# Kernel tuning notes

Measured on AMD Instinct MI355X. Metric: run time of the kernel, lower is better.

The kernel has to match this reference:

```python
import jax, jax.numpy as jnp
import numpy as np

B, H, W, C, F, K = 64, 56, 56, 256, 256, 3


def _conv(x, w, padding):
    # NHWC input, HWIO kernel, stride 1
    return jax.lax.conv_general_dilated(
        x, w, window_strides=(1, 1), padding=padding,
        dimension_numbers=('NHWC', 'HWIO', 'NHWC'))


def setup_inputs() -> dict:
    key = jax.random.key(0)
    kx, kw = jax.random.split(key)
    x = jax.random.normal(kx, (B, H, W, C), dtype=jnp.float32)
    stdv = 1.0 / np.sqrt(K * K * C)  # matches build()'s init scale
    w = (jax.random.normal(kw, (K, K, C, F), dtype=jnp.float32) * stdv).astype(jnp.float32)
    return {"x": x, "w": w}


def reference(x, w):
    # fp16_grad forward: round-trip weights through fp16
    wq = w.astype(jnp.float16).astype(jnp.float32)
    # binarize_weight forward value: sign(clip(w, -1, 1))
    wb = jnp.sign(jnp.clip(wq, -1.0, 1.0))
    return _conv(x, wb, 'SAME')
```

## Files before the change

kernel.cpp:

```cpp
#include <hip/hip_runtime.h>
#include <hip/hip_bf16.h>
#include <hip/hip_fp16.h>

typedef __bf16 bf16x8 __attribute__((ext_vector_type(8)));
typedef float  f32x4  __attribute__((ext_vector_type(4)));

#define C_H 56
#define C_W 56
#define C_C 256
#define C_F 256
#define C_B 64
#define N_PIX (C_B * C_H * C_W)
#define WB_ELEMS (9 * C_C * C_F)
#define WB_BYTES (WB_ELEMS * 2)
#define ZBUF_BYTES 1024
#define XB_OFF (WB_BYTES + ZBUF_BYTES)
#define X_ELEMS (N_PIX * C_C)

#define GLOAD_LDS16(g, l)                                                   \
    __builtin_amdgcn_global_load_lds(                                        \
        (const __attribute__((address_space(1))) void*)(g),                  \
        (__attribute__((address_space(3))) void*)(l), 16, 0, 0)

__global__ void prep_w_kernel(const float* __restrict__ w, __bf16* __restrict__ wbT) {
    int idx = blockIdx.x * 256 + threadIdx.x;
    int f = idx & 255;
    int c = (idx >> 8) & 255;
    int s = idx >> 16;
    float wf = w[idx];
    float v = __half2float(__float2half(wf));
    float sgn = (v > 0.f) ? 1.f : ((v < 0.f) ? -1.f : 0.f);
    wbT[(s << 16) + (f << 8) + c] = (__bf16)sgn;
}

__global__ void zero_kernel(float* __restrict__ z) {
    z[threadIdx.x] = 0.f;
}

__global__ void prep_x_kernel(const float* __restrict__ x, __bf16* __restrict__ xb) {
    int i = blockIdx.x * 256 + threadIdx.x;
    const f32x4* p = reinterpret_cast<const f32x4*>(x) + (size_t)i * 2;
    f32x4 a = p[0], b = p[1];
    bf16x8 o;
    o[0] = (__bf16)a[0]; o[1] = (__bf16)a[1]; o[2] = (__bf16)a[2]; o[3] = (__bf16)a[3];
    o[4] = (__bf16)b[0]; o[5] = (__bf16)b[1]; o[6] = (__bf16)b[2]; o[7] = (__bf16)b[3];
    reinterpret_cast<bf16x8*>(xb)[i] = o;
}

__global__ __launch_bounds__(512, 2) void conv_mfma8_kernel(
    const char* __restrict__ xbp,
    const char* __restrict__ wbp,
    const char* __restrict__ zp,
    float* __restrict__ out) {

    __shared__ __align__(16) char sm[4][32768];

    const int nbid = (blockIdx.x & 7) * 98 + (blockIdx.x >> 3);
    const long m0 = (long)nbid * 256;

    const int tid  = threadIdx.x;
    const int lane = tid & 63;
    const int wave = tid >> 6;
    const int l15  = lane & 15;
    const int g4   = lane >> 4;
    const int wm   = wave >> 2;
    const int wn   = wave & 3;
    const int colr = ((g4 ^ (l15 & 3)) << 4);

    const int r0 = tid >> 2;
    const int sw = (((tid & 3) << 4)) ^ ((r0 & 3) << 4);
    const int p0 = (int)m0 + r0;
    const int p1 = p0 + 128;
    const int rem0 = p0 % 3136;
    const int rem1 = p1 % 3136;
    const int y0 = rem0 / 56, x0 = rem0 - (rem0 / 56) * 56;
    const int y1 = rem1 / 56, x1 = rem1 - (rem1 / 56) * 56;

    auto stage = [&](int kts) {
        int cc = (kts * 57) >> 9;
        int s  = kts - 9 * cc;
        int s3 = (s * 171) >> 9;
        int dy = s3 - 1;
        int dx = s - 3 * s3 - 1;
        int doff = dy * 56 + dx;
        size_t cb = (size_t)(cc << 6) + sw;
        bool v0 = ((unsigned)(y0 + dy) < 56u) & ((unsigned)(x0 + dx) < 56u);
        bool v1 = ((unsigned)(y1 + dy) < 56u) & ((unsigned)(x1 + dx) < 56u);
        const char* a0 = v0 ? xbp + (size_t)(p0 + doff) * 512 + cb : zp + sw;
        const char* a1 = v1 ? xbp + (size_t)(p1 + doff) * 512 + cb : zp + sw;
        const char* b0 = wbp + (size_t)((s << 8) + r0) * 512 + cb;
        const char* b1 = wbp + (size_t)((s << 8) + r0 + 128) * 512 + cb;
        char* L = &sm[kts & 3][0];
        GLOAD_LDS16(a0, L + tid * 16);
        GLOAD_LDS16(a1, L + 8192 + tid * 16);
        GLOAD_LDS16(b0, L + 16384 + tid * 16);
        GLOAD_LDS16(b1, L + 24576 + tid * 16);
    };

    f32x4 acc[8][4];
#pragma unroll
    for (int i = 0; i < 8; ++i)
#pragma unroll
        for (int j = 0; j < 4; ++j)
            acc[i][j] = (f32x4){0.f, 0.f, 0.f, 0.f};

    auto body = [&](int t, bool do_stage) {
        const char* L = &sm[t & 3][0];
        const char* Ab = L + (size_t)(wm * 128 + l15) * 64 + colr;
        const char* Bb = L + 16384 + (size_t)(wn * 64 + l15) * 64 + colr;
        bf16x8 Af[8], Bf[4];
#pragma unroll
        for (int ai = 0; ai < 8; ++ai)
            Af[ai] = *reinterpret_cast<const bf16x8*>(Ab + ai * 1024);
#pragma unroll
        for (int bj = 0; bj < 4; ++bj)
            Bf[bj] = *reinterpret_cast<const bf16x8*>(Bb + bj * 1024);
        if (do_stage) stage(t + 3);
        __builtin_amdgcn_s_setprio(1);
#pragma unroll
        for (int ai = 0; ai < 8; ++ai)
#pragma unroll
            for (int bj = 0; bj < 4; ++bj)
                acc[ai][bj] = __builtin_amdgcn_mfma_f32_16x16x32_bf16(
                    Af[ai], Bf[bj], acc[ai][bj], 0, 0, 0);
        __builtin_amdgcn_s_setprio(0);
    };

    stage(0); stage(1); stage(2);

    for (int t = 0; t < 69; ++t) {
        asm volatile("s_waitcnt vmcnt(8)" ::: "memory");
        __builtin_amdgcn_s_barrier();
        __builtin_amdgcn_sched_barrier(0);
        body(t, true);
    }
    asm volatile("s_waitcnt vmcnt(8)" ::: "memory");
    __builtin_amdgcn_s_barrier();
    __builtin_amdgcn_sched_barrier(0);
    body(69, false);
    asm volatile("s_waitcnt vmcnt(4)" ::: "memory");
    __builtin_amdgcn_s_barrier();
    __builtin_amdgcn_sched_barrier(0);
    body(70, false);
    asm volatile("s_waitcnt vmcnt(0)" ::: "memory");
    __builtin_amdgcn_s_barrier();
    __builtin_amdgcn_sched_barrier(0);
    body(71, false);

#pragma unroll
    for (int ai = 0; ai < 8; ++ai) {
#pragma unroll
        for (int j = 0; j < 4; ++j) {
            long row = m0 + wm * 128 + ai * 16 + g4 * 4 + j;
            float* op = out + row * C_F + wn * 64 + l15;
#pragma unroll
            for (int bj = 0; bj < 4; ++bj)
                op[bj * 16] = acc[ai][bj][j];
        }
    }
}

__global__ __launch_bounds__(256) void conv_fallback_kernel(
    const float* __restrict__ xf,
    const __bf16* __restrict__ wbT, const char* __restrict__ zbuf,
    float* __restrict__ out) {

    const int lane = threadIdx.x & 63;
    const int wave = threadIdx.x >> 6;
    const int l15  = lane & 15;
    const int g    = lane >> 4;
    const int goff = g * 8;
    const long m0  = (long)blockIdx.x * 64;
    const int fbase = wave * 64;

    int ry[4], rx[4];
    long rbase[4];
#pragma unroll
    for (int ai = 0; ai < 4; ++ai) {
        int rr = (int)m0 + ai * 16 + l15;
        int b = rr / 3136;
        int rem = rr - b * 3136;
        int yy2 = rem / 56;
        ry[ai] = yy2;
        rx[ai] = rem - yy2 * 56;
        rbase[ai] = (long)rr * C_C;
    }

    f32x4 acc[4][4];
#pragma unroll
    for (int i = 0; i < 4; ++i)
#pragma unroll
        for (int j = 0; j < 4; ++j)
            acc[i][j] = (f32x4){0.f, 0.f, 0.f, 0.f};

    for (int s = 0; s < 9; ++s) {
        const int dy = s / 3 - 1;
        const int dx = (s - (s / 3) * 3) - 1;
        const float* af[4];
#pragma unroll
        for (int ai = 0; ai < 4; ++ai) {
            bool v = ((unsigned)(ry[ai] + dy) < 56u) & ((unsigned)(rx[ai] + dx) < 56u);
            long off = rbase[ai] + (long)(dy * C_W + dx) * C_C + goff;
            af[ai] = v ? (xf + off) : ((const float*)zbuf + goff);
        }
        const __bf16* bp = wbT + ((size_t)(s * 256 + fbase + l15)) * C_C + goff;

#pragma unroll
        for (int cc = 0; cc < 8; ++cc) {
            const int c0 = cc * 32;
            bf16x8 A[4], Bf[4];
#pragma unroll
            for (int ai = 0; ai < 4; ++ai) {
                const f32x4* p = reinterpret_cast<const f32x4*>(af[ai] + c0);
                f32x4 u = p[0], w2 = p[1];
                bf16x8 t;
                t[0] = (__bf16)u[0]; t[1] = (__bf16)u[1]; t[2] = (__bf16)u[2]; t[3] = (__bf16)u[3];
                t[4] = (__bf16)w2[0]; t[5] = (__bf16)w2[1]; t[6] = (__bf16)w2[2]; t[7] = (__bf16)w2[3];
                A[ai] = t;
            }
#pragma unroll
            for (int bj = 0; bj < 4; ++bj)
                Bf[bj] = *reinterpret_cast<const bf16x8*>(bp + bj * 16 * C_C + c0);
#pragma unroll
            for (int ai = 0; ai < 4; ++ai)
#pragma unroll
                for (int bj = 0; bj < 4; ++bj)
                    acc[ai][bj] = __builtin_amdgcn_mfma_f32_16x16x32_bf16(A[ai], Bf[bj], acc[ai][bj], 0, 0, 0);
        }
    }

#pragma unroll
    for (int ai = 0; ai < 4; ++ai) {
#pragma unroll
        for (int j = 0; j < 4; ++j) {
            long row = m0 + ai * 16 + g * 4 + j;
            float* op = out + row * C_F + fbase + l15;
#pragma unroll
            for (int bj = 0; bj < 4; ++bj)
                op[bj * 16] = acc[ai][bj][j];
        }
    }
}

extern "C" void kernel_launch(void* const* d_in, const int* in_sizes, int n_in,
                              void* d_out, int out_size, void* d_ws, size_t ws_size,
                              hipStream_t stream) {
    const float* x = (const float*)d_in[0];
    const float* w = (const float*)d_in[1];
    float* out = (float*)d_out;

    char* ws = (char*)d_ws;
    __bf16* wbT = (__bf16*)ws;
    char* zbuf = ws + WB_BYTES;
    __bf16* xb = (__bf16*)(ws + XB_OFF);

    const bool prex = ws_size >= (size_t)XB_OFF + (size_t)X_ELEMS * 2;

    prep_w_kernel<<<WB_ELEMS / 256, 256, 0, stream>>>(w, wbT);
    zero_kernel<<<1, 256, 0, stream>>>((float*)zbuf);

    if (prex) {
        prep_x_kernel<<<X_ELEMS / 8 / 256, 256, 0, stream>>>(x, xb);
        conv_mfma8_kernel<<<N_PIX / 256, 512, 0, stream>>>(
            (const char*)xb, (const char*)wbT, zbuf, out);
    } else {
        conv_fallback_kernel<<<N_PIX / 64, 256, 0, stream>>>(x, wbT, zbuf, out);
    }
}
```

Baseline: 344.4 us.

## Prefetch next K-tile LDS fragments during MFMAs and change LDS swizzle

Restructures the main loop so LDS reads for the next K-step are interleaved with the current step's MFMA instructions, using double-buffered B fragment registers and an unrolled-by-two loop. It also changes the XOR swizzle of the LDS layout to use bits 1-2 of the row index, aiming to reduce bank conflicts on the ds_read pattern. The aim is to hide LDS read latency behind matrix work. In exchange it raises register pressure under the 2-blocks-per-CU launch bound and relies on hand-tuned waitcnt values.

Measured after the change: 319.4 us. -7.3%, faster.

```diff
diff --git a/kernel.cpp b/kernel.cpp
--- a/kernel.cpp
+++ b/kernel.cpp
@@ -65,10 +65,12 @@
     const int g4   = lane >> 4;
     const int wm   = wave >> 2;
     const int wn   = wave & 3;
-    const int colr = ((g4 ^ (l15 & 3)) << 4);
+    const int colr = ((g4 ^ ((l15 >> 1) & 3)) << 4);
+    const int rdA = (wm * 128 + l15) * 64 + colr;
+    const int rdB = 16384 + (wn * 64 + l15) * 64 + colr;
 
     const int r0 = tid >> 2;
-    const int sw = (((tid & 3) << 4)) ^ ((r0 & 3) << 4);
+    const int sw = ((tid & 3) ^ ((r0 >> 1) & 3)) << 4;
     const int p0 = (int)m0 + r0;
     const int p1 = p0 + 128;
     const int rem0 = p0 % 3136;
@@ -76,9 +78,9 @@
     const int y0 = rem0 / 56, x0 = rem0 - (rem0 / 56) * 56;
     const int y1 = rem1 / 56, x1 = rem1 - (rem1 / 56) * 56;
 
-    auto stage = [&](int kts) {
-        int cc = (kts * 57) >> 9;
-        int s  = kts - 9 * cc;
+    auto stage = [&](int kt) {
+        int cc = (kt * 57) >> 9;
+        int s  = kt - 9 * cc;
         int s3 = (s * 171) >> 9;
         int dy = s3 - 1;
         int dx = s - 3 * s3 - 1;
@@ -90,7 +92,7 @@
         const char* a1 = v1 ? xbp + (size_t)(p1 + doff) * 512 + cb : zp + sw;
         const char* b0 = wbp + (size_t)((s << 8) + r0) * 512 + cb;
         const char* b1 = wbp + (size_t)((s << 8) + r0 + 128) * 512 + cb;
-        char* L = &sm[kts & 3][0];
+        char* L = &sm[kt & 3][0];
         GLOAD_LDS16(a0, L + tid * 16);
         GLOAD_LDS16(a1, L + 8192 + tid * 16);
         GLOAD_LDS16(b0, L + 16384 + tid * 16);
@@ -104,48 +106,64 @@
         for (int j = 0; j < 4; ++j)
             acc[i][j] = (f32x4){0.f, 0.f, 0.f, 0.f};
 
-    auto body = [&](int t, bool do_stage) {
-        const char* L = &sm[t & 3][0];
-        const char* Ab = L + (size_t)(wm * 128 + l15) * 64 + colr;
-        const char* Bb = L + 16384 + (size_t)(wn * 64 + l15) * 64 + colr;
-        bf16x8 Af[8], Bf[4];
-#pragma unroll
-        for (int ai = 0; ai < 8; ++ai)
-            Af[ai] = *reinterpret_cast<const bf16x8*>(Ab + ai * 1024);
-#pragma unroll
-        for (int bj = 0; bj < 4; ++bj)
-            Bf[bj] = *reinterpret_cast<const bf16x8*>(Bb + bj * 1024);
-        if (do_stage) stage(t + 3);
-        __builtin_amdgcn_s_setprio(1);
-#pragma unroll
-        for (int ai = 0; ai < 8; ++ai)
-#pragma unroll
-            for (int bj = 0; bj < 4; ++bj)
-                acc[ai][bj] = __builtin_amdgcn_mfma_f32_16x16x32_bf16(
-                    Af[ai], Bf[bj], acc[ai][bj], 0, 0, 0);
-        __builtin_amdgcn_s_setprio(0);
-    };
-
-    stage(0); stage(1); stage(2);
-
-    for (int t = 0; t < 69; ++t) {
-        asm volatile("s_waitcnt vmcnt(8)" ::: "memory");
+    bf16x8 Af[8], Bx[4], By[4];
+
+    auto body = [&](int t, bf16x8 (&Bc)[4], bf16x8 (&Bn)[4], bool doStage, bool doPre) {
         __builtin_amdgcn_s_barrier();
         __builtin_amdgcn_sched_barrier(0);
-        body(t, true);
-    }
+        if (doStage) stage(t + 3);
+        const char* L1 = &sm[(t + 1) & 3][0];
+        const char* Ab = L1 + rdA;
+        const char* Bb = L1 + rdB;
+        __builtin_amdgcn_s_setprio(1);
+#pragma unroll
+        for (int ai = 0; ai < 8; ++ai) {
+#pragma unroll
+            for (int bj = 0; bj < 4; ++bj)
+                acc[ai][bj] = __builtin_amdgcn_mfma_f32_16x16x32_bf16(
+                    Af[ai], Bc[bj], acc[ai][bj], 0, 0, 0);
+            if (doPre)
+                Af[ai] = *reinterpret_cast<const bf16x8*>(Ab + ai * 1024);
+        }
+        __builtin_amdgcn_s_setprio(0);
+        if (doPre) {
+#pragma unroll
+            for (int bj = 0; bj < 4; ++bj)
+                Bn[bj] = *reinterpret_cast<const bf16x8*>(Bb + bj * 1024);
+            asm volatile("s_waitcnt lgkmcnt(12)" ::: "memory");
+            __builtin_amdgcn_sched_barrier(0);
+        }
+    };
+
+    stage(0); stage(1); stage(2);
     asm volatile("s_waitcnt vmcnt(8)" ::: "memory");
     __builtin_amdgcn_s_barrier();
     __builtin_amdgcn_sched_barrier(0);
-    body(69, false);
+    {
+        const char* L0 = &sm[0][0];
+#pragma unroll
+        for (int ai = 0; ai < 8; ++ai)
+            Af[ai] = *reinterpret_cast<const bf16x8*>(L0 + rdA + ai * 1024);
+#pragma unroll
+        for (int bj = 0; bj < 4; ++bj)
+            Bx[bj] = *reinterpret_cast<const bf16x8*>(L0 + rdB + bj * 1024);
+    }
+    asm volatile("s_waitcnt lgkmcnt(0)" ::: "memory");
+    __builtin_amdgcn_sched_barrier(0);
+
+    for (int tt = 0; tt < 68; tt += 2) {
+        asm volatile("s_waitcnt vmcnt(4)" ::: "memory");
+        body(tt, Bx, By, true, true);
+        asm volatile("s_waitcnt vmcnt(4)" ::: "memory");
+        body(tt + 1, By, Bx, true, true);
+    }
     asm volatile("s_waitcnt vmcnt(4)" ::: "memory");
-    __builtin_amdgcn_s_barrier();
-    __builtin_amdgcn_sched_barrier(0);
-    body(70, false);
+    body(68, Bx, By, true, true);
+    asm volatile("s_waitcnt vmcnt(4)" ::: "memory");
+    body(69, By, Bx, false, true);
     asm volatile("s_waitcnt vmcnt(0)" ::: "memory");
-    __builtin_amdgcn_s_barrier();
-    __builtin_amdgcn_sched_barrier(0);
-    body(71, false);
+    body(70, Bx, By, false, true);
+    body(71, By, Bx, false, false);
 
 #pragma unroll
     for (int ai = 0; ai < 8; ++ai) {
```
